# Kernel tuning notes

Measured on AMD Instinct MI355X. Metric: run time of the kernel, lower is better.

The kernel has to match this reference:

```python
import jax, jax.numpy as jnp
import numpy as np

B, C, H, W = 32, 256, 64, 64
LN_EPS = 1e-5

def _conv1x1(x, w, b=None):
    # x: (b,c,h,w), w: (out,c) -> (b,out,h,w)
    y = jnp.einsum('bchw,oc->bohw', x, w)
    if b is not None:
        y = y + b[None, :, None, None]
    return y

def _hsigmoid(t):
    # mmcv HSigmoid: clamp((x + 3) / 6, 0, 1)
    return jnp.clip((t + 3.0) / 6.0, 0.0, 1.0)

def setup_inputs() -> dict:
    key = jax.random.key(0)
    ks = jax.random.split(key, 12)
    s = 0.05
    return {
        'x': jax.random.normal(ks[0], (B, C, H, W), jnp.float32),
        'conv0_w': jax.random.normal(ks[1], (C // 2, C), jnp.float32) * s,
        'conv0_b': jnp.zeros((C // 2,), jnp.float32),
        'bn1_w': jax.random.normal(ks[2], (C, C // 2), jnp.float32) * s,
        'bn1_b': jnp.zeros((C,), jnp.float32),
        'conv1_w': jax.random.normal(ks[3], (1, C), jnp.float32) * s,
        'conv1_b': jnp.zeros((1,), jnp.float32),
        'ln_g': jnp.ones((C,), jnp.float32),
        'ln_b': jnp.zeros((C,), jnp.float32),
        'sk_w1': jax.random.normal(ks[4], (C // 2, C), jnp.float32) * s,
        'sk_w2': jax.random.normal(ks[5], (C, C // 2), jnp.float32) * s,
        'res_w': jax.random.normal(ks[6], (C, C), jnp.float32) * s,
        'res_b': jnp.zeros((C,), jnp.float32),
    }

def reference(x, conv0_w, conv0_b, bn1_w, bn1_b, conv1_w, conv1_b,
              ln_g, ln_b, sk_w1, sk_w2, res_w, res_b):
    b, c, h, w = x.shape
    # ---- channel attention ----
    ca = _conv1x1(x, conv0_w, conv0_b)               # (b, c/2, h, w)
    ca = ca.mean(axis=(2, 3), keepdims=True)          # GAP -> (b, c/2, 1, 1)
    ca = _conv1x1(ca, bn1_w, bn1_b)                   # (b, c, 1, 1)
    ca = _hsigmoid(ca)
    v = ca.reshape(b, c)                              # nchw_to_nlc -> (b, 1, c); LN over c
    mu = v.mean(axis=-1, keepdims=True)
    var = ((v - mu) ** 2).mean(axis=-1, keepdims=True)
    v = (v - mu) * jax.lax.rsqrt(var + LN_EPS) * ln_g + ln_b
    ca = v.reshape(b, c, 1, 1)
    # ---- spatial attention ----
    sa = _conv1x1(x, conv1_w, conv1_b)                # (b, 1, h, w)
    # ---- parallel attention ----
    par = _hsigmoid(sa + ca)                          # (b, c, h, w)
    # ---- sequence attention: bmm outer product (b,c,1)x(b,1,hw) ----
    seq = _hsigmoid(ca * sa)                          # (b, c, h, w)
    # ---- SK module ----
    u = (seq + par).mean(axis=(2, 3), keepdims=True)  # GAP -> (b, c, 1, 1)
    u = _conv1x1(u, sk_w1)                            # (b, c/2, 1, 1), no bias
    u = _conv1x1(u, sk_w2)                            # (b, c, 1, 1), no bias
    a = jax.nn.softmax(u, axis=1)
    sk = seq * a + par * (1.0 - a)
    # softmax over spatial (nchw_to_nlc + Softmax(dim=1))
    sk = jax.nn.softmax(sk.reshape(b, c, h * w), axis=2).reshape(b, c, h, w)
    selected = x * sk
    # ---- self attention ----
    self_attn = selected.sum(axis=(2, 3)).reshape(b, c, 1, 1) + _conv1x1(x, res_w, res_b)
    return selected + self_attn
```

## Files before the change

### kernel.cpp

```cpp
#include <hip/hip_runtime.h>
#include <math.h>

#define B_  32
#define C_  256
#define HW_ 4096
#define LN_EPS 1e-5f

typedef __attribute__((ext_vector_type(4))) float f32x4;
typedef __attribute__((ext_vector_type(8))) short bf16x8;
typedef __attribute__((ext_vector_type(4))) unsigned u32x4;
typedef __attribute__((ext_vector_type(2))) unsigned u32x2;

__device__ __forceinline__ float hsig(float v) {
    return fminf(fmaxf((v + 3.0f) * (1.0f / 6.0f), 0.0f), 1.0f);
}
__device__ __forceinline__ float tval(float ca, float a, float sav) {
    return a * hsig(ca * sav) + (1.0f - a) * hsig(ca + sav);
}
__device__ __forceinline__ unsigned short f2bf(float f) {
    unsigned u = __float_as_uint(f);
    unsigned r = (u + 0x7fffu + ((u >> 16) & 1u)) >> 16;
    return (unsigned short)r;
}
__device__ __forceinline__ float bf2f(unsigned short h) {
    return __uint_as_float(((unsigned)h) << 16);
}
__device__ __forceinline__ int bswz(int n) {
    return ((n & 7) ^ ((n >> 3) & 7)) << 4;
}


__global__ __launch_bounds__(1024) void k_pass1d(
    const float* __restrict__ x, const float* __restrict__ w1,
    float* __restrict__ sa, unsigned short* __restrict__ xbf)
{
    __shared__ float sw1[C_];
    __shared__ float sred[16][512];
    int hwq = blockIdx.x, b = blockIdx.y;
    int tid = threadIdx.x, w = tid >> 6, l = tid & 63;
    int hw0 = hwq * 512;
    if (tid < 256) sw1[tid] = w1[tid];
    __syncthreads();
    const float* xb = x + (size_t)b * (C_ * HW_) + hw0 + l * 8;
    unsigned short* xo = xbf + (size_t)b * (C_ * HW_) + hw0 + l * 8;
    f32x4 s0 = {0.f, 0.f, 0.f, 0.f}, s1 = {0.f, 0.f, 0.f, 0.f};
    #pragma unroll 4
    for (int i = 0; i < 16; ++i) {
        int c = i * 16 + w;
        const float* p = xb + (size_t)c * HW_;
        f32x4 v0 = *(const f32x4*)p;
        f32x4 v1 = *(const f32x4*)(p + 4);
        float wv = sw1[c];
        s0 += wv * v0;
        s1 += wv * v1;
        u32x4 o;
        o[0] = (unsigned)f2bf(v0.x) | ((unsigned)f2bf(v0.y) << 16);
        o[1] = (unsigned)f2bf(v0.z) | ((unsigned)f2bf(v0.w) << 16);
        o[2] = (unsigned)f2bf(v1.x) | ((unsigned)f2bf(v1.y) << 16);
        o[3] = (unsigned)f2bf(v1.z) | ((unsigned)f2bf(v1.w) << 16);
        *(u32x4*)(xo + (size_t)c * HW_) = o;
    }
    *(f32x4*)&sred[w][l * 8] = s0;
    *(f32x4*)&sred[w][l * 8 + 4] = s1;
    __syncthreads();
    if (tid < 512) {
        float s = 0.f;
        #pragma unroll
        for (int g = 0; g < 16; ++g) s += sred[g][tid];
        sa[(size_t)b * HW_ + hw0 + tid] = s;
    }
}

__global__ void k_xs(const unsigned short* __restrict__ xbf, float* __restrict__ xs) {
    int bc = blockIdx.x;
    int l = threadIdx.x;
    const u32x4* p = (const u32x4*)(xbf + (size_t)bc * HW_);
    float s = 0.f;
    #pragma unroll
    for (int i = 0; i < 8; ++i) {
        u32x4 v = p[i * 64 + l];
        #pragma unroll
        for (int j = 0; j < 4; ++j) {
            s += bf2f((unsigned short)(v[j] & 0xffffu));
            s += bf2f((unsigned short)(v[j] >> 16));
        }
    }
    #pragma unroll
    for (int o = 32; o; o >>= 1) s += __shfl_xor(s, o);
    if (l == 0) xs[bc] = s;
}

__global__ void k_ca(const float* __restrict__ xs_part, const float* __restrict__ w0,
                     const float* __restrict__ b0, const float* __restrict__ w1,
                     const float* __restrict__ b1, const float* __restrict__ g,
                     const float* __restrict__ be, float* __restrict__ ca,
                     const float* __restrict__ rw, unsigned short* __restrict__ wbs,
                     int nparts) {
    int b = blockIdx.x, tid = threadIdx.x;
    __shared__ float xm[C_], t0[128], red[4];
    float xs = 0.f;
    for (int i = 0; i < nparts; ++i)
        xs += xs_part[((size_t)i * B_ + b) * C_ + tid];
    xm[tid] = xs * (1.0f / HW_);
    __syncthreads();
    if (tid < 128) {
        float s = b0[tid];
        const float* wr = w0 + tid * C_;
        for (int c = 0; c < C_; ++c) s += wr[c] * xm[c];
        t0[tid] = s;
    }
    __syncthreads();
    float s = b1[tid];
    const float* wr = w1 + tid * 128;
    for (int o = 0; o < 128; ++o) s += wr[o] * t0[o];
    float v = hsig(s);
    float sum = v;
    #pragma unroll
    for (int o = 32; o; o >>= 1) sum += __shfl_xor(sum, o);
    if ((tid & 63) == 0) red[tid >> 6] = sum;
    __syncthreads();
    float mu = (red[0] + red[1] + red[2] + red[3]) * (1.0f / C_);
    __syncthreads();
    float d = v - mu;
    float sq = d * d;
    #pragma unroll
    for (int o = 32; o; o >>= 1) sq += __shfl_xor(sq, o);
    if ((tid & 63) == 0) red[tid >> 6] = sq;
    __syncthreads();
    float var = (red[0] + red[1] + red[2] + red[3]) * (1.0f / C_);
    ca[b * C_ + tid] = d * (1.0f / sqrtf(var + LN_EPS)) * g[tid] + be[tid];

    int gid = b * 256 + tid;
    int lane = gid & 63;
    int mi = (gid >> 6) & 3;
    int ks = (gid >> 8) & 7;
    int wv2 = gid >> 11;
    int m = wv2 * 64 + mi * 16 + (lane & 15);
    int kb = ks * 32 + (lane >> 4) * 8;
    const float* src = rw + m * C_ + kb;
    f32x4 a4 = *(const f32x4*)src;
    f32x4 b4 = *(const f32x4*)(src + 4);
    ushort4 o0 = { f2bf(a4.x), f2bf(a4.y), f2bf(a4.z), f2bf(a4.w) };
    ushort4 o1 = { f2bf(b4.x), f2bf(b4.y), f2bf(b4.z), f2bf(b4.w) };
    unsigned short* dst = wbs + (size_t)gid * 8;
    *(ushort4*)dst = o0;
    *(ushort4*)(dst + 4) = o1;
}

__global__ void k_u(const float* __restrict__ sa, const float* __restrict__ ca,
                    const float* __restrict__ b1, float* __restrict__ u) {
    int bc = blockIdx.x;
    int b = bc >> 8;
    int tid = threadIdx.x;
    float cav = ca[bc];
    float bias = b1[0];
    const float* sp = sa + (size_t)b * HW_;
    float s = 0.f;
    for (int i = 0; i < 16; ++i) {
        f32x4 v = *(const f32x4*)(sp + i * 256 + tid * 4);
        #pragma unroll
        for (int j = 0; j < 4; ++j) {
            float sv = v[j] + bias;
            s += hsig(cav * sv) + hsig(cav + sv);
        }
    }
    #pragma unroll
    for (int o = 32; o; o >>= 1) s += __shfl_xor(s, o);
    if (tid == 0) u[bc] = s * (1.0f / HW_);
}

__global__ void k_a(const float* __restrict__ u, const float* __restrict__ w1,
                    const float* __restrict__ w2, float* __restrict__ aout) {
    int b = blockIdx.x, tid = threadIdx.x;
    __shared__ float uu[C_], v0[128], red[4];
    uu[tid] = u[b * C_ + tid];
    __syncthreads();
    if (tid < 128) {
        float s = 0.f;
        const float* wr = w1 + tid * C_;
        for (int c = 0; c < C_; ++c) s += wr[c] * uu[c];
        v0[tid] = s;
    }
    __syncthreads();
    float s = 0.f;
    const float* wr = w2 + tid * 128;
    for (int o = 0; o < 128; ++o) s += wr[o] * v0[o];
    float m = s;
    #pragma unroll
    for (int o = 32; o; o >>= 1) m = fmaxf(m, __shfl_xor(m, o));
    if ((tid & 63) == 0) red[tid >> 6] = m;
    __syncthreads();
    m = fmaxf(fmaxf(red[0], red[1]), fmaxf(red[2], red[3]));
    __syncthreads();
    float e = __expf(s - m);
    float se = e;
    #pragma unroll
    for (int o = 32; o; o >>= 1) se += __shfl_xor(se, o);
    if ((tid & 63) == 0) red[tid >> 6] = se;
    __syncthreads();
    float tot = red[0] + red[1] + red[2] + red[3];
    aout[b * C_ + tid] = e / tot;
}

__global__ void k_stats3(const unsigned short* __restrict__ xbf, const float* __restrict__ sa,
                         const float* __restrict__ b1,
                         const float* __restrict__ ca, const float* __restrict__ aw,
                         const float* __restrict__ res_b, f32x4* __restrict__ st4) {
    int bc = blockIdx.x;
    int b = bc >> 8, c = bc & 255;
    int tid = threadIdx.x;
    float cav = ca[bc], av = aw[bc];
    float bias = b1[0];
    const float* sp = sa + (size_t)b * HW_;
    const unsigned* xp = (const unsigned*)(xbf + (size_t)bc * HW_);
    float se = 0.f, xe = 0.f;
    #pragma unroll
    for (int i = 0; i < 4; ++i) {
        f32x4 s4 = *(const f32x4*)(sp + i * 1024 + tid * 4);
        u32x2 x2 = *(const u32x2*)(xp + i * 512 + tid * 2);
        float xv[4];
        xv[0] = bf2f((unsigned short)(x2[0] & 0xffffu));
        xv[1] = bf2f((unsigned short)(x2[0] >> 16));
        xv[2] = bf2f((unsigned short)(x2[1] & 0xffffu));
        xv[3] = bf2f((unsigned short)(x2[1] >> 16));
        #pragma unroll
        for (int j = 0; j < 4; ++j) {
            float e = __expf(tval(cav, av, s4[j] + bias));
            se += e;
            xe += xv[j] * e;
        }
    }
    __shared__ float red[4], red2[4];
    #pragma unroll
    for (int o = 32; o; o >>= 1) { se += __shfl_xor(se, o); xe += __shfl_xor(xe, o); }
    if ((tid & 63) == 0) { red[tid >> 6] = se; red2[tid >> 6] = xe; }
    __syncthreads();
    if (tid == 0) {
        float S = red[0] + red[1] + red[2] + red[3];
        float X = red2[0] + red2[1] + red2[2] + red2[3];
        float rcp = 1.0f / S;
        f32x4 st = { cav, av, rcp, X * rcp + res_b[c] };
        st4[bc] = st;
    }
}

__global__ __launch_bounds__(256, 3) void k_out3(
    const unsigned short* __restrict__ xbf, const unsigned short* __restrict__ wbs,
    const float* __restrict__ sa, const float* __restrict__ b1,
    const f32x4* __restrict__ st4, float* __restrict__ out)
{
    __shared__ __align__(16) unsigned short Bs[64 * 256];
    __shared__ f32x4 sst[C_];
    __shared__ float ssa[64];

    int b = blockIdx.x, tile = blockIdx.y;
    int n0 = tile * 64;
    int tid = threadIdx.x;
    int w = tid >> 6, lane = tid & 63;
    int hwc = tid & 7;
    int cq  = tid >> 3;

    const unsigned short* xb = xbf + (size_t)b * (C_ * HW_) + n0 + hwc * 8;
    u32x4 ld[2][4];
    #pragma unroll
    for (int it = 0; it < 2; ++it) {
        int c0 = it * 128 + cq * 4;
        #pragma unroll
        for (int r = 0; r < 4; ++r)
            ld[it][r] = *(const u32x4*)(xb + (size_t)(c0 + r) * HW_);
    }

    bf16x8 af[2][4];
    const bf16x8* wp = (const bf16x8*)wbs;
    #pragma unroll
    for (int ks2 = 0; ks2 < 2; ++ks2)
        #pragma unroll
        for (int mi = 0; mi < 4; ++mi)
            af[ks2][mi] = wp[(size_t)(((w * 8 + ks2) * 4 + mi) * 64 + lane)];

    sst[tid] = st4[b * C_ + tid];
    if (tid < 64) ssa[tid] = sa[(size_t)b * HW_ + n0 + tid] + b1[0];

    #pragma unroll
    for (int it = 0; it < 2; ++it) {
        int kp0 = it * 64 + cq * 2;
        #pragma unroll
        for (int e = 0; e < 8; ++e) {
            int n = hwc * 8 + e;
            unsigned a0 = ld[it][0][e >> 1], b0v = ld[it][1][e >> 1];
            unsigned a1 = ld[it][2][e >> 1], b1v = ld[it][3][e >> 1];
            unsigned d0, d1;
            if (e & 1) {
                d0 = (a0 >> 16) | (b0v & 0xffff0000u);
                d1 = (a1 >> 16) | (b1v & 0xffff0000u);
            } else {
                d0 = (a0 & 0xffffu) | (b0v << 16);
                d1 = (a1 & 0xffffu) | (b1v << 16);
            }
            int bo = (n * 512 + kp0 * 4) ^ bswz(n);
            u32x2 dd = { d0, d1 };
            *(u32x2*)((char*)Bs + bo) = dd;
        }
    }
    __syncthreads();

    f32x4 acc[4][4];
    #pragma unroll
    for (int i = 0; i < 4; ++i)
        #pragma unroll
        for (int j = 0; j < 4; ++j) acc[i][j] = (f32x4){0.f, 0.f, 0.f, 0.f};

    #pragma unroll
    for (int ksg = 0; ksg < 4; ++ksg) {
        #pragma unroll
        for (int ks2 = 0; ks2 < 2; ++ks2) {
            int ks = ksg * 2 + ks2;
            bf16x8 bfr[4];
            #pragma unroll
            for (int ni = 0; ni < 4; ++ni) {
                int n = ni * 16 + (lane & 15);
                int bo = (n * 512 + ks * 64 + (lane >> 4) * 16) ^ bswz(n);
                bfr[ni] = *(const bf16x8*)((const char*)Bs + bo);
            }
            #pragma unroll
            for (int mi = 0; mi < 4; ++mi)
                #pragma unroll
                for (int ni = 0; ni < 4; ++ni)
                    acc[mi][ni] = __builtin_amdgcn_mfma_f32_16x16x32_bf16(
                        af[ks2][mi], bfr[ni], acc[mi][ni], 0, 0, 0);
            if (ksg < 3) {
                #pragma unroll
                for (int mi = 0; mi < 4; ++mi)
                    af[ks2][mi] = wp[(size_t)(((w * 8 + (ksg + 1) * 2 + ks2) * 4 + mi) * 64 + lane)];
            }
        }
    }

    float* ob = out + (size_t)b * (C_ * HW_) + n0;
    #pragma unroll
    for (int mi = 0; mi < 4; ++mi) {
        int m0 = w * 64 + mi * 16 + (lane >> 4) * 4;
        f32x4 s0 = sst[m0 + 0];
        f32x4 s1 = sst[m0 + 1];
        f32x4 s2 = sst[m0 + 2];
        f32x4 s3 = sst[m0 + 3];
        #pragma unroll
        for (int ni = 0; ni < 4; ++ni) {
            int n = ni * 16 + (lane & 15);
            float sav = ssa[n];
            int bo = (n * 512 + m0 * 2) ^ bswz(n);
            ushort4 xv = *(const ushort4*)((const char*)Bs + bo);
            float o0 = acc[mi][ni][0] + bf2f(xv.x) * (__expf(tval(s0.x, s0.y, sav)) * s0.z) + s0.w;
            float o1 = acc[mi][ni][1] + bf2f(xv.y) * (__expf(tval(s1.x, s1.y, sav)) * s1.z) + s1.w;
            float o2 = acc[mi][ni][2] + bf2f(xv.z) * (__expf(tval(s2.x, s2.y, sav)) * s2.z) + s2.w;
            float o3 = acc[mi][ni][3] + bf2f(xv.w) * (__expf(tval(s3.x, s3.y, sav)) * s3.z) + s3.w;
            ob[(size_t)(m0 + 0) * HW_ + n] = o0;
            ob[(size_t)(m0 + 1) * HW_ + n] = o1;
            ob[(size_t)(m0 + 2) * HW_ + n] = o2;
            ob[(size_t)(m0 + 3) * HW_ + n] = o3;
        }
    }
}


__global__ void k_pass1(const float* __restrict__ x, const float* __restrict__ w1,
                        float* __restrict__ sa, float* __restrict__ xs_part)
{
    int tid = threadIdx.x, wave = tid >> 6, lane = tid & 63;
    int hwq = blockIdx.x, b = blockIdx.y, ct = blockIdx.z;
    int c0 = ct * 32;
    int hw0 = hwq * 1024;
    const float* xb = x + (size_t)b * (C_ * HW_) + hw0 + tid * 4;
    __shared__ float part[32 * 4];
    f32x4 sacc = {0.f, 0.f, 0.f, 0.f};
    #pragma unroll 4
    for (int cc = 0; cc < 32; ++cc) {
        int c = c0 + cc;
        f32x4 v = *(const f32x4*)(xb + (size_t)c * HW_);
        float wv = w1[c];
        sacc += wv * v;
        float h = (v.x + v.y) + (v.z + v.w);
        h += __shfl_xor(h, 32); h += __shfl_xor(h, 16); h += __shfl_xor(h, 8);
        h += __shfl_xor(h, 4);  h += __shfl_xor(h, 2);  h += __shfl_xor(h, 1);
        if (lane == 0) part[cc * 4 + wave] = h;
    }
    float* sp = sa + (size_t)b * HW_ + hw0 + tid * 4;
    atomicAdd(sp + 0, sacc.x);
    atomicAdd(sp + 1, sacc.y);
    atomicAdd(sp + 2, sacc.z);
    atomicAdd(sp + 3, sacc.w);
    __syncthreads();
    if (tid < 32)
        xs_part[((size_t)hwq * B_ + b) * C_ + c0 + tid] =
            part[tid * 4 + 0] + part[tid * 4 + 1] + part[tid * 4 + 2] + part[tid * 4 + 3];
}

__global__ void k_stats(const float* __restrict__ x, const float* __restrict__ sa,
                        const float* __restrict__ b1,
                        const float* __restrict__ ca, const float* __restrict__ aw,
                        const float* __restrict__ res_b, f32x4* __restrict__ st4) {
    int bc = blockIdx.x;
    int b = bc >> 8, c = bc & 255;
    int tid = threadIdx.x;
    float cav = ca[bc], av = aw[bc];
    float bias = b1[0];
    const float* sp = sa + (size_t)b * HW_;
    const float* xp = x + (size_t)bc * HW_;
    float se = 0.f, xe = 0.f;
    #pragma unroll
    for (int i = 0; i < 4; ++i) {
        f32x4 s4 = *(const f32x4*)(sp + i * 1024 + tid * 4);
        f32x4 x4 = *(const f32x4*)(xp + i * 1024 + tid * 4);
        #pragma unroll
        for (int j = 0; j < 4; ++j) {
            float e = __expf(tval(cav, av, s4[j] + bias));
            se += e;
            xe += x4[j] * e;
        }
    }
    __shared__ float red[4], red2[4];
    #pragma unroll
    for (int o = 32; o; o >>= 1) { se += __shfl_xor(se, o); xe += __shfl_xor(xe, o); }
    if ((tid & 63) == 0) { red[tid >> 6] = se; red2[tid >> 6] = xe; }
    __syncthreads();
    if (tid == 0) {
        float S = red[0] + red[1] + red[2] + red[3];
        float X = red2[0] + red2[1] + red2[2] + red2[3];
        float rcp = 1.0f / S;
        f32x4 st = { cav, av, rcp, X * rcp + res_b[c] };
        st4[bc] = st;
    }
}

__global__ __launch_bounds__(256, 2) void k_out(
    const float* __restrict__ x, const unsigned short* __restrict__ wbs,
    const float* __restrict__ sa, const float* __restrict__ b1,
    const f32x4* __restrict__ st4, float* __restrict__ out)
{
    __shared__ __align__(16) unsigned short Bs[64 * 256];
    __shared__ f32x4 sst[C_];
    __shared__ float ssa[64];

    int b = blockIdx.x, tile = blockIdx.y;
    int n0 = tile * 64;
    int tid = threadIdx.x;
    int w = tid >> 6, lane = tid & 63;

    const float* xb = x + (size_t)b * (C_ * HW_);

    bf16x8 af[8][4];
    #pragma unroll
    for (int ks = 0; ks < 8; ++ks)
        #pragma unroll
        for (int mi = 0; mi < 4; ++mi)
            af[ks][mi] = *(const bf16x8*)(wbs + (size_t)(((w * 8 + ks) * 4 + mi) * 64 + lane) * 8);

    sst[tid] = st4[b * C_ + tid];
    if (tid < 64) ssa[tid] = sa[(size_t)b * HW_ + n0 + tid] + b1[0];

    #pragma unroll
    for (int p2 = 0; p2 < 8; ++p2) {
        int id = p2 * 256 + tid;
        int kp = id >> 4;
        int tcn = id & 15;
        const float* g0 = xb + (size_t)(2 * kp) * HW_ + n0 + 4 * tcn;
        f32x4 v0 = *(const f32x4*)g0;
        f32x4 v1 = *(const f32x4*)(g0 + HW_);
        #pragma unroll
        for (int i = 0; i < 4; ++i) {
            int n = 4 * tcn + i;
            unsigned val = (unsigned)f2bf(v0[i]) | ((unsigned)f2bf(v1[i]) << 16);
            int bo = (n * 512 + kp * 4) ^ ((n & 7) << 4);
            *(unsigned*)((char*)Bs + bo) = val;
        }
    }
    __syncthreads();

    f32x4 acc[4][4];
    #pragma unroll
    for (int i = 0; i < 4; ++i)
        #pragma unroll
        for (int j = 0; j < 4; ++j) acc[i][j] = (f32x4){0.f, 0.f, 0.f, 0.f};

    #pragma unroll
    for (int ks = 0; ks < 8; ++ks) {
        bf16x8 bfr[4];
        #pragma unroll
        for (int ni = 0; ni < 4; ++ni) {
            int n = ni * 16 + (lane & 15);
            int bo = (n * 512 + ks * 64 + (lane >> 4) * 16) ^ ((n & 7) << 4);
            bfr[ni] = *(const bf16x8*)((const char*)Bs + bo);
        }
        #pragma unroll
        for (int mi = 0; mi < 4; ++mi)
            #pragma unroll
            for (int ni = 0; ni < 4; ++ni)
                acc[mi][ni] = __builtin_amdgcn_mfma_f32_16x16x32_bf16(
                    af[ks][mi], bfr[ni], acc[mi][ni], 0, 0, 0);
    }

    float* ob = out + (size_t)b * (C_ * HW_) + n0;
    #pragma unroll
    for (int mi = 0; mi < 4; ++mi) {
        int m0 = w * 64 + mi * 16 + (lane >> 4) * 4;
        f32x4 s0 = sst[m0 + 0];
        f32x4 s1 = sst[m0 + 1];
        f32x4 s2 = sst[m0 + 2];
        f32x4 s3 = sst[m0 + 3];
        #pragma unroll
        for (int ni = 0; ni < 4; ++ni) {
            int n = ni * 16 + (lane & 15);
            float sav = ssa[n];
            int bo = (n * 512 + m0 * 2) ^ ((n & 7) << 4);
            ushort4 xv = *(const ushort4*)((const char*)Bs + bo);
            float o0 = acc[mi][ni][0] + bf2f(xv.x) * (__expf(tval(s0.x, s0.y, sav)) * s0.z) + s0.w;
            float o1 = acc[mi][ni][1] + bf2f(xv.y) * (__expf(tval(s1.x, s1.y, sav)) * s1.z) + s1.w;
            float o2 = acc[mi][ni][2] + bf2f(xv.z) * (__expf(tval(s2.x, s2.y, sav)) * s2.z) + s2.w;
            float o3 = acc[mi][ni][3] + bf2f(xv.w) * (__expf(tval(s3.x, s3.y, sav)) * s3.z) + s3.w;
            ob[(size_t)(m0 + 0) * HW_ + n] = o0;
            ob[(size_t)(m0 + 1) * HW_ + n] = o1;
            ob[(size_t)(m0 + 2) * HW_ + n] = o2;
            ob[(size_t)(m0 + 3) * HW_ + n] = o3;
        }
    }
}

extern "C" void kernel_launch(void* const* d_in, const int* in_sizes, int n_in,
                              void* d_out, int out_size, void* d_ws, size_t ws_size,
                              hipStream_t stream) {
    (void)in_sizes; (void)n_in; (void)out_size;
    const float* x   = (const float*)d_in[0];
    const float* c0w = (const float*)d_in[1];
    const float* c0b = (const float*)d_in[2];
    const float* b1w = (const float*)d_in[3];
    const float* b1b = (const float*)d_in[4];
    const float* c1w = (const float*)d_in[5];
    const float* c1b = (const float*)d_in[6];
    const float* lng = (const float*)d_in[7];
    const float* lnb = (const float*)d_in[8];
    const float* sw1 = (const float*)d_in[9];
    const float* sw2 = (const float*)d_in[10];
    const float* rw  = (const float*)d_in[11];
    const float* rb  = (const float*)d_in[12];
    float* out = (float*)d_out;
    float* ws = (float*)d_ws;

    const size_t NEW_WS_FLOATS = (size_t)352256 + 16777216;
    if (ws_size >= NEW_WS_FLOATS * sizeof(float)) {
        float* sa      = ws;
        float* xs_part = ws + 131072;
        float* ca      = ws + 262144;
        float* u       = ws + 270336;
        float* aw      = ws + 278528;
        f32x4* st4     = (f32x4*)(ws + 286720);
        unsigned short* wbs = (unsigned short*)(ws + 319488);
        unsigned short* xbf = (unsigned short*)(ws + 352256);

        hipLaunchKernelGGL(k_pass1d, dim3(8, 32),  dim3(1024), 0, stream, x, c1w, sa, xbf);
        hipLaunchKernelGGL(k_xs,     dim3(8192),   dim3(64),   0, stream, xbf, xs_part);
        hipLaunchKernelGGL(k_ca,     dim3(32),     dim3(256),  0, stream, xs_part, c0w, c0b, b1w, b1b, lng, lnb, ca, rw, wbs, 1);
        hipLaunchKernelGGL(k_u,      dim3(8192),   dim3(64),   0, stream, sa, ca, c1b, u);
        hipLaunchKernelGGL(k_a,      dim3(32),     dim3(256),  0, stream, u, sw1, sw2, aw);
        hipLaunchKernelGGL(k_stats3, dim3(8192),   dim3(256),  0, stream, xbf, sa, c1b, ca, aw, rb, st4);
        hipLaunchKernelGGL(k_out3,   dim3(32, 64), dim3(256),  0, stream, xbf, wbs, sa, c1b, st4, out);
    } else {
        float* sa      = ws;
        float* xs_part = ws + 131072;
        float* ca      = ws + 163840;
        float* u       = ws + 172032;
        float* aw      = ws + 180224;
        f32x4* st4     = (f32x4*)(ws + 188416);
        unsigned short* wbs = (unsigned short*)(ws + 221184);

        hipMemsetAsync(sa, 0, (size_t)B_ * HW_ * sizeof(float), stream);
        hipLaunchKernelGGL(k_pass1, dim3(4, 32, 8), dim3(256), 0, stream, x, c1w, sa, xs_part);
        hipLaunchKernelGGL(k_ca,    dim3(32),       dim3(256), 0, stream, xs_part, c0w, c0b, b1w, b1b, lng, lnb, ca, rw, wbs, 4);
        hipLaunchKernelGGL(k_u,     dim3(8192),     dim3(64),  0, stream, sa, ca, c1b, u);
        hipLaunchKernelGGL(k_a,     dim3(32),       dim3(256), 0, stream, u, sw1, sw2, aw);
        hipLaunchKernelGGL(k_stats, dim3(8192),     dim3(256), 0, stream, x, sa, c1b, ca, aw, rb, st4);
        hipLaunchKernelGGL(k_out,   dim3(32, 64),   dim3(256), 0, stream, x, wbs, sa, c1b, st4, out);
    }
}
```

Measured before the change: 161.7 us.

## Fuse channel-sum into pass1 and process two channels per block in u/stats

Per-channel spatial sums are now computed inside the first pass with wavefront shuffles, written as 8 partial buffers, and the separate k_xs kernel that re-read the bf16 copy of x is removed. k_u and k_stats each now handle two channels per block, so the shared sa row is loaded once for two channels and half as many blocks are launched. The cost is extra shuffle work in the bandwidth-bound first pass, 8-way partial summation in k_ca, and a channel sum taken from fp32 values rather than the bf16 copy.

```diff
diff --git a/kernel.cpp b/kernel.cpp
--- a/kernel.cpp
+++ b/kernel.cpp
@@ -30,12 +30,14 @@
 }
 
 
-__global__ __launch_bounds__(1024) void k_pass1d(
+__global__ __launch_bounds__(1024) void k_pass1e(
     const float* __restrict__ x, const float* __restrict__ w1,
-    float* __restrict__ sa, unsigned short* __restrict__ xbf)
+    float* __restrict__ sa, float* __restrict__ xs_part,
+    unsigned short* __restrict__ xbf)
 {
     __shared__ float sw1[C_];
     __shared__ float sred[16][512];
+    __shared__ float xsl[C_];
     int hwq = blockIdx.x, b = blockIdx.y;
     int tid = threadIdx.x, w = tid >> 6, l = tid & 63;
     int hw0 = hwq * 512;
@@ -59,6 +61,10 @@
         o[2] = (unsigned)f2bf(v1.x) | ((unsigned)f2bf(v1.y) << 16);
         o[3] = (unsigned)f2bf(v1.z) | ((unsigned)f2bf(v1.w) << 16);
         *(u32x4*)(xo + (size_t)c * HW_) = o;
+        float h = ((v0.x + v0.y) + (v0.z + v0.w)) + ((v1.x + v1.y) + (v1.z + v1.w));
+        h += __shfl_xor(h, 32); h += __shfl_xor(h, 16); h += __shfl_xor(h, 8);
+        h += __shfl_xor(h, 4);  h += __shfl_xor(h, 2);  h += __shfl_xor(h, 1);
+        if (l == 0) xsl[c] = h;
     }
     *(f32x4*)&sred[w][l * 8] = s0;
     *(f32x4*)&sred[w][l * 8 + 4] = s1;
@@ -69,25 +75,7 @@
         for (int g = 0; g < 16; ++g) s += sred[g][tid];
         sa[(size_t)b * HW_ + hw0 + tid] = s;
     }
-}
-
-__global__ void k_xs(const unsigned short* __restrict__ xbf, float* __restrict__ xs) {
-    int bc = blockIdx.x;
-    int l = threadIdx.x;
-    const u32x4* p = (const u32x4*)(xbf + (size_t)bc * HW_);
-    float s = 0.f;
-    #pragma unroll
-    for (int i = 0; i < 8; ++i) {
-        u32x4 v = p[i * 64 + l];
-        #pragma unroll
-        for (int j = 0; j < 4; ++j) {
-            s += bf2f((unsigned short)(v[j] & 0xffffu));
-            s += bf2f((unsigned short)(v[j] >> 16));
-        }
-    }
-    #pragma unroll
-    for (int o = 32; o; o >>= 1) s += __shfl_xor(s, o);
-    if (l == 0) xs[bc] = s;
+    if (tid < 256) xs_part[((size_t)hwq * B_ + b) * C_ + tid] = xsl[tid];
 }
 
 __global__ void k_ca(const float* __restrict__ xs_part, const float* __restrict__ w0,
@@ -147,26 +135,30 @@
     *(ushort4*)(dst + 4) = o1;
 }
 
-__global__ void k_u(const float* __restrict__ sa, const float* __restrict__ ca,
-                    const float* __restrict__ b1, float* __restrict__ u) {
+__global__ void k_u2(const float* __restrict__ sa, const float* __restrict__ ca,
+                     const float* __restrict__ b1, float* __restrict__ u) {
     int bc = blockIdx.x;
-    int b = bc >> 8;
+    int b = bc >> 7, c0 = (bc & 127) * 2;
     int tid = threadIdx.x;
-    float cav = ca[bc];
+    float ca0 = ca[b * C_ + c0], ca1 = ca[b * C_ + c0 + 1];
     float bias = b1[0];
     const float* sp = sa + (size_t)b * HW_;
-    float s = 0.f;
+    float s0 = 0.f, s1 = 0.f;
     for (int i = 0; i < 16; ++i) {
         f32x4 v = *(const f32x4*)(sp + i * 256 + tid * 4);
         #pragma unroll
         for (int j = 0; j < 4; ++j) {
             float sv = v[j] + bias;
-            s += hsig(cav * sv) + hsig(cav + sv);
-        }
-    }
-    #pragma unroll
-    for (int o = 32; o; o >>= 1) s += __shfl_xor(s, o);
-    if (tid == 0) u[bc] = s * (1.0f / HW_);
+            s0 += hsig(ca0 * sv) + hsig(ca0 + sv);
+            s1 += hsig(ca1 * sv) + hsig(ca1 + sv);
+        }
+    }
+    #pragma unroll
+    for (int o = 32; o; o >>= 1) { s0 += __shfl_xor(s0, o); s1 += __shfl_xor(s1, o); }
+    if (tid == 0) {
+        u[b * C_ + c0]     = s0 * (1.0f / HW_);
+        u[b * C_ + c0 + 1] = s1 * (1.0f / HW_);
+    }
 }
 
 __global__ void k_a(const float* __restrict__ u, const float* __restrict__ w1,
@@ -202,45 +194,65 @@
     aout[b * C_ + tid] = e / tot;
 }
 
-__global__ void k_stats3(const unsigned short* __restrict__ xbf, const float* __restrict__ sa,
+__global__ void k_stats4(const unsigned short* __restrict__ xbf, const float* __restrict__ sa,
                          const float* __restrict__ b1,
                          const float* __restrict__ ca, const float* __restrict__ aw,
                          const float* __restrict__ res_b, f32x4* __restrict__ st4) {
-    int bc = blockIdx.x;
-    int b = bc >> 8, c = bc & 255;
+    int blk = blockIdx.x;
+    int b = blk >> 7, c0 = (blk & 127) * 2;
+    int bc0 = b * C_ + c0;
     int tid = threadIdx.x;
-    float cav = ca[bc], av = aw[bc];
+    float ca0 = ca[bc0],     a0 = aw[bc0];
+    float ca1 = ca[bc0 + 1], a1 = aw[bc0 + 1];
     float bias = b1[0];
     const float* sp = sa + (size_t)b * HW_;
-    const unsigned* xp = (const unsigned*)(xbf + (size_t)bc * HW_);
-    float se = 0.f, xe = 0.f;
+    const unsigned* xp0 = (const unsigned*)(xbf + (size_t)bc0 * HW_);
+    const unsigned* xp1 = (const unsigned*)(xbf + (size_t)(bc0 + 1) * HW_);
+    float se0 = 0.f, xe0 = 0.f, se1 = 0.f, xe1 = 0.f;
     #pragma unroll
     for (int i = 0; i < 4; ++i) {
         f32x4 s4 = *(const f32x4*)(sp + i * 1024 + tid * 4);
-        u32x2 x2 = *(const u32x2*)(xp + i * 512 + tid * 2);
-        float xv[4];
-        xv[0] = bf2f((unsigned short)(x2[0] & 0xffffu));
-        xv[1] = bf2f((unsigned short)(x2[0] >> 16));
-        xv[2] = bf2f((unsigned short)(x2[1] & 0xffffu));
-        xv[3] = bf2f((unsigned short)(x2[1] >> 16));
+        u32x2 xa = *(const u32x2*)(xp0 + i * 512 + tid * 2);
+        u32x2 xc = *(const u32x2*)(xp1 + i * 512 + tid * 2);
+        float va[4], vc[4];
+        va[0] = bf2f((unsigned short)(xa[0] & 0xffffu));
+        va[1] = bf2f((unsigned short)(xa[0] >> 16));
+        va[2] = bf2f((unsigned short)(xa[1] & 0xffffu));
+        va[3] = bf2f((unsigned short)(xa[1] >> 16));
+        vc[0] = bf2f((unsigned short)(xc[0] & 0xffffu));
+        vc[1] = bf2f((unsigned short)(xc[0] >> 16));
+        vc[2] = bf2f((unsigned short)(xc[1] & 0xffffu));
+        vc[3] = bf2f((unsigned short)(xc[1] >> 16));
         #pragma unroll
         for (int j = 0; j < 4; ++j) {
-            float e = __expf(tval(cav, av, s4[j] + bias));
-            se += e;
-            xe += xv[j] * e;
-        }
-    }
-    __shared__ float red[4], red2[4];
-    #pragma unroll
-    for (int o = 32; o; o >>= 1) { se += __shfl_xor(se, o); xe += __shfl_xor(xe, o); }
-    if ((tid & 63) == 0) { red[tid >> 6] = se; red2[tid >> 6] = xe; }
+            float sv = s4[j] + bias;
+            float e0 = __expf(tval(ca0, a0, sv));
+            float e1 = __expf(tval(ca1, a1, sv));
+            se0 += e0; xe0 += va[j] * e0;
+            se1 += e1; xe1 += vc[j] * e1;
+        }
+    }
+    __shared__ float red[4][4];
+    #pragma unroll
+    for (int o = 32; o; o >>= 1) {
+        se0 += __shfl_xor(se0, o); xe0 += __shfl_xor(xe0, o);
+        se1 += __shfl_xor(se1, o); xe1 += __shfl_xor(xe1, o);
+    }
+    if ((tid & 63) == 0) {
+        int w = tid >> 6;
+        red[0][w] = se0; red[1][w] = xe0; red[2][w] = se1; red[3][w] = xe1;
+    }
     __syncthreads();
     if (tid == 0) {
-        float S = red[0] + red[1] + red[2] + red[3];
-        float X = red2[0] + red2[1] + red2[2] + red2[3];
-        float rcp = 1.0f / S;
-        f32x4 st = { cav, av, rcp, X * rcp + res_b[c] };
-        st4[bc] = st;
+        float S0 = red[0][0] + red[0][1] + red[0][2] + red[0][3];
+        float X0 = red[1][0] + red[1][1] + red[1][2] + red[1][3];
+        float S1 = red[2][0] + red[2][1] + red[2][2] + red[2][3];
+        float X1 = red[3][0] + red[3][1] + red[3][2] + red[3][3];
+        float r0 = 1.0f / S0, r1 = 1.0f / S1;
+        f32x4 st0 = { ca0, a0, r0, X0 * r0 + res_b[c0] };
+        f32x4 st1 = { ca1, a1, r1, X1 * r1 + res_b[c0 + 1] };
+        st4[bc0] = st0;
+        st4[bc0 + 1] = st1;
     }
 }
 
@@ -395,6 +407,28 @@
             part[tid * 4 + 0] + part[tid * 4 + 1] + part[tid * 4 + 2] + part[tid * 4 + 3];
 }
 
+__global__ void k_u(const float* __restrict__ sa, const float* __restrict__ ca,
+                    const float* __restrict__ b1, float* __restrict__ u) {
+    int bc = blockIdx.x;
+    int b = bc >> 8;
+    int tid = threadIdx.x;
+    float cav = ca[bc];
+    float bias = b1[0];
+    const float* sp = sa + (size_t)b * HW_;
+    float s = 0.f;
+    for (int i = 0; i < 16; ++i) {
+        f32x4 v = *(const f32x4*)(sp + i * 256 + tid * 4);
+        #pragma unroll
+        for (int j = 0; j < 4; ++j) {
+            float sv = v[j] + bias;
+            s += hsig(cav * sv) + hsig(cav + sv);
+        }
+    }
+    #pragma unroll
+    for (int o = 32; o; o >>= 1) s += __shfl_xor(s, o);
+    if (tid == 0) u[bc] = s * (1.0f / HW_);
+}
+
 __global__ void k_stats(const float* __restrict__ x, const float* __restrict__ sa,
                         const float* __restrict__ b1,
                         const float* __restrict__ ca, const float* __restrict__ aw,
@@ -556,12 +590,11 @@
         unsigned short* wbs = (unsigned short*)(ws + 319488);
         unsigned short* xbf = (unsigned short*)(ws + 352256);
 
-        hipLaunchKernelGGL(k_pass1d, dim3(8, 32),  dim3(1024), 0, stream, x, c1w, sa, xbf);
-        hipLaunchKernelGGL(k_xs,     dim3(8192),   dim3(64),   0, stream, xbf, xs_part);
-        hipLaunchKernelGGL(k_ca,     dim3(32),     dim3(256),  0, stream, xs_part, c0w, c0b, b1w, b1b, lng, lnb, ca, rw, wbs, 1);
-        hipLaunchKernelGGL(k_u,      dim3(8192),   dim3(64),   0, stream, sa, ca, c1b, u);
+        hipLaunchKernelGGL(k_pass1e, dim3(8, 32),  dim3(1024), 0, stream, x, c1w, sa, xs_part, xbf);
+        hipLaunchKernelGGL(k_ca,     dim3(32),     dim3(256),  0, stream, xs_part, c0w, c0b, b1w, b1b, lng, lnb, ca, rw, wbs, 8);
+        hipLaunchKernelGGL(k_u2,     dim3(4096),   dim3(64),   0, stream, sa, ca, c1b, u);
         hipLaunchKernelGGL(k_a,      dim3(32),     dim3(256),  0, stream, u, sw1, sw2, aw);
-        hipLaunchKernelGGL(k_stats3, dim3(8192),   dim3(256),  0, stream, xbf, sa, c1b, ca, aw, rb, st4);
+        hipLaunchKernelGGL(k_stats4, dim3(4096),   dim3(256),  0, stream, xbf, sa, c1b, ca, aw, rb, st4);
         hipLaunchKernelGGL(k_out3,   dim3(32, 64), dim3(256),  0, stream, xbf, wbs, sa, c1b, st4, out);
     } else {
         float* sa      = ws;
```

Result: faster. 154.6 us (-4.4%).
